# Kernel optimization log

Hardware: AMD Instinct MI355X
Metric: run time of the kernel (lower is better)

Reference implementation:

```python
import jax, jax.numpy as jnp
import numpy as np

EPS_Q = 1e-5
EPS_RMS = 1e-6


def _bitlinear(x, w):
    # absmean ternary weight quantization with STE (STE irrelevant for fwd)
    w_scale = jnp.maximum(jnp.mean(jnp.abs(w)), EPS_Q)
    w_q = jnp.clip(jnp.round(w / w_scale), -1.0, 1.0)
    w_q = jax.lax.stop_gradient(w_q - w) + w
    # per-token absmax activation quantization
    x_scale = jnp.maximum(jnp.max(jnp.abs(x), axis=-1, keepdims=True), EPS_Q)
    x_s = x / x_scale
    out = jnp.einsum('bi,oi->bo', x_s, w_q)
    return out * x_scale


def _rmsnorm(x, g):
    rms = jnp.sqrt(jnp.mean(x * x, axis=-1, keepdims=True) + EPS_RMS)
    return x / rms * g


def setup_inputs() -> dict:
    key = jax.random.key(0)
    ks = jax.random.split(key, 6)
    B, IN, H, OUT = 65536, 784, 1024, 10
    return {
        'x': jax.random.normal(ks[0], (B, IN), dtype=jnp.float32),
        'w1': jax.random.normal(ks[1], (H, IN), dtype=jnp.float32) * 0.02,
        'g1': jnp.ones((H,), dtype=jnp.float32),
        'w2': jax.random.normal(ks[2], (H, H), dtype=jnp.float32) * 0.02,
        'g2': jnp.ones((H,), dtype=jnp.float32),
        'w3': jax.random.normal(ks[3], (OUT, H), dtype=jnp.float32) * 0.02,
    }


def reference(x, w1, g1, w2, g2, w3):
    h = _bitlinear(x, w1)
    h = jax.nn.gelu(_rmsnorm(h, g1), approximate=False)
    h = _bitlinear(h, w2)
    h = jax.nn.gelu(_rmsnorm(h, g2), approximate=False)
    return _bitlinear(h, w3)
```

## Files before the change

### kernel.cpp

```cpp
#include <hip/hip_runtime.h>
#include <hip/hip_bf16.h>
#include <stdint.h>


typedef __attribute__((ext_vector_type(8))) short short8;
typedef __attribute__((ext_vector_type(4))) float f32x4;

#define B_TOTAL 65536
#define IN_DIM 784
#define IN_PAD 832
#define H_DIM 1024
#define OUT_DIM 10
#define OUT_PAD 16

__device__ __forceinline__ unsigned short f2bf(float f) {
    union { float f; unsigned u; } c; c.f = f;
    unsigned r = c.u + 0x7FFFu + ((c.u >> 16) & 1u);
    return (unsigned short)(r >> 16);
}
__device__ __forceinline__ float bf2f(unsigned short h) {
    union { unsigned u; float f; } c; c.u = ((unsigned)h) << 16;
    return c.f;
}

__device__ __forceinline__ float gelu_fast(float t) {
    const float z = t * 0.70710678118f;
    const float s = fabsf(z);
    const float tt = 1.0f / (1.0f + 0.3275911f * s);
    const float e = __expf(-s * s);
    float p = fmaf(tt, 1.061405429f, -1.453152027f);
    p = fmaf(tt, p, 1.421413741f);
    p = fmaf(tt, p, -0.284496736f);
    p = fmaf(tt, p, 0.254829592f);
    float erfa = fmaf(-p * tt, e, 1.0f);
    erfa = copysignf(erfa, z);
    return 0.5f * t * (1.0f + erfa);
}

#define GLOAD16(gp, lp)                                                        \
    __builtin_amdgcn_global_load_lds(                                          \
        (const __attribute__((address_space(1))) void*)(gp),                   \
        (__attribute__((address_space(3))) void*)(lp), 16, 0, 0)

__global__ void absum3_kernel(const float* __restrict__ w1, const float* __restrict__ w2,
                              const float* __restrict__ w3, double* acc) {
    __shared__ float red[4];
    const int which = blockIdx.y;
    const float* w = (which == 0) ? w1 : (which == 1) ? w2 : w3;
    const int n = (which == 0) ? H_DIM * IN_DIM : (which == 1) ? H_DIM * H_DIM : OUT_DIM * H_DIM;
    float s = 0.f;
    for (int i = blockIdx.x * blockDim.x + threadIdx.x; i < n; i += gridDim.x * blockDim.x)
        s += fabsf(w[i]);
#pragma unroll
    for (int o = 32; o > 0; o >>= 1) s += __shfl_xor(s, o);
    if ((threadIdx.x & 63) == 0) red[threadIdx.x >> 6] = s;
    __syncthreads();
    if (threadIdx.x == 0) {
        float t = red[0] + red[1] + red[2] + red[3];
        atomicAdd(acc + which, (double)t);
    }
}

__global__ void quant_all(const float* __restrict__ w1, const float* __restrict__ w2,
                          const float* __restrict__ w3,
                          unsigned short* __restrict__ w1q, unsigned short* __restrict__ w2q,
                          unsigned short* __restrict__ w3q, const double* sums) {
    const int k = blockIdx.x * blockDim.x + threadIdx.x;
    const int y = blockIdx.y;
    const float* w; unsigned short* wq; int o, O, K, Kp, n; const double* sum;
    if (y < 1024)      { w = w1; wq = w1q; o = y;        O = H_DIM;  K = IN_DIM; Kp = IN_PAD; n = H_DIM * IN_DIM;  sum = sums + 0; }
    else if (y < 2048) { w = w2; wq = w2q; o = y - 1024; O = H_DIM;  K = H_DIM;  Kp = H_DIM;  n = H_DIM * H_DIM;  sum = sums + 1; }
    else               { w = w3; wq = w3q; o = y - 2048; O = OUT_DIM; K = H_DIM; Kp = H_DIM;  n = OUT_DIM * H_DIM; sum = sums + 2; }
    if (k >= Kp) return;
    float scale = fmaxf((float)(*sum / (double)n), 1e-5f);
    float q = 0.f;
    if (o < O && k < K) {
        float r = rintf(w[(size_t)o * K + k] / scale);
        q = fminf(1.f, fmaxf(-1.f, r));
    }
    wq[(size_t)o * Kp + k] = f2bf(q);
}

__global__ __launch_bounds__(256)
void convert_pad(const float* __restrict__ x, unsigned short* __restrict__ xb) {
    const int g = blockIdx.x * 256 + threadIdx.x;
    const int row = g / 104;
    const int c = (g % 104) * 8;
    short8 v = 0;
    if (c < IN_DIM) {
        const float* p = x + (size_t)row * IN_DIM + c;
        float4 f0 = *(const float4*)p;
        float4 f1 = *(const float4*)(p + 4);
        v[0] = (short)f2bf(f0.x); v[1] = (short)f2bf(f0.y);
        v[2] = (short)f2bf(f0.z); v[3] = (short)f2bf(f0.w);
        v[4] = (short)f2bf(f1.x); v[5] = (short)f2bf(f1.y);
        v[6] = (short)f2bf(f1.z); v[7] = (short)f2bf(f1.w);
    }
    *(short8*)(xb + (size_t)row * IN_PAD + c) = v;
}

template<int KP>
__global__ __launch_bounds__(512, 2)
void gemm_bt(const unsigned short* __restrict__ A, const unsigned short* __restrict__ Bq,
             unsigned short* __restrict__ C) {
    constexpr int NT = KP / 64;
    __shared__ __attribute__((aligned(16))) unsigned short LDS[65536];
    const int tid = threadIdx.x;
    const int lane = tid & 63;
    const int w = tid >> 6;
    const int wm = w >> 2, wn = w & 3;
    const int lr = lane & 15, gq = lane >> 4;
    const int gsw8 = (gq ^ ((lr >> 3) << 1)) * 8;
    const int lrO = lr * 32;
    const int bid = blockIdx.x;
    const int xcd = bid & 7, slot = bid >> 3;
    const int nblk = slot & 3;
    const int mblk = xcd * (gridDim.x >> 5) + (slot >> 2);
    const int m0 = mblk * 256, n0 = nblk * 256;
    const int rS = lane >> 2;
    const int cS = ((lane & 3) ^ ((lane >> 5) << 1)) * 8;
    const int stA0 = w;
    const int stA1 = 8 + w;
    const int stB_P1 = (w >> 2) * 8 + (w & 3);
    const int stB_P3 = stB_P1 + 4;

#define STG(gbase, areaS, st)                                                  \
    {   const unsigned short* _g = (gbase) +                                   \
            (size_t)(((st) >> 1) * 16 + rS) * KP + ((st) & 1) * 32 + cS;       \
        GLOAD16(_g, &LDS[(areaS) + (st) * 512]);                               \
        GLOAD16(_g + (size_t)128 * KP, &LDS[(areaS) + (st) * 512 + 8192]); }
#define RD_A(mq, mf, kk)                                                       \
    (*(const short8*)&LDS[curS + ((wm * 8 + (mq) * 4 + (mf)) * 2 + (kk)) * 512 + lrO + gsw8])
#define RD_B(nq, nf, kk)                                                       \
    (*(const short8*)&LDS[curS + 16384 + ((wn * 4 + (nq) * 2 + (nf)) * 2 + (kk)) * 512 + lrO + gsw8])
#define MM(mq, nq, mf, nf, kk)                                                 \
    acc[(mq) * 4 + (mf)][(nq) * 2 + (nf)] =                                    \
        __builtin_amdgcn_mfma_f32_16x16x32_bf16(af[mf][kk], bf[nf][kk],        \
            acc[(mq) * 4 + (mf)][(nq) * 2 + (nf)], 0, 0, 0)

    f32x4 acc[8][4] = {};
    short8 af[4][2], bf[2][2];
    STG(A + (size_t)m0 * KP, 0, stA0);
    STG(Bq + (size_t)n0 * KP, 16384, stB_P1);
    STG(Bq + (size_t)n0 * KP, 16384, stB_P3);
    STG(A + (size_t)m0 * KP, 0, stA1);
    STG(A + (size_t)m0 * KP + 64, 32768, stA0);
    STG(Bq + (size_t)n0 * KP + 64, 49152, stB_P3);
    STG(A + (size_t)m0 * KP + 64, 32768, stA1);
    asm volatile("s_waitcnt vmcnt(6)" ::: "memory");
#pragma unroll 2
    for (int t = 0; t < NT; ++t) {
        const int curS = (t & 1) * 32768;
        const int nxtS = curS ^ 32768;
        __builtin_amdgcn_s_barrier();
        af[0][0] = RD_A(0, 0, 0); bf[0][0] = RD_B(0, 0, 0);
        af[1][0] = RD_A(0, 1, 0); bf[1][0] = RD_B(0, 1, 0);
        __builtin_amdgcn_s_setprio(1);
        MM(0, 0, 0, 0, 0); af[2][0] = RD_A(0, 2, 0);
        MM(0, 0, 0, 1, 0); af[3][0] = RD_A(0, 3, 0);
        MM(0, 0, 1, 0, 0); af[0][1] = RD_A(0, 0, 1);
        MM(0, 0, 1, 1, 0); bf[0][1] = RD_B(0, 0, 1);
        MM(0, 0, 2, 0, 0); af[1][1] = RD_A(0, 1, 1);
        MM(0, 0, 2, 1, 0); bf[1][1] = RD_B(0, 1, 1);
        MM(0, 0, 3, 0, 0); af[2][1] = RD_A(0, 2, 1);
        MM(0, 0, 3, 1, 0); af[3][1] = RD_A(0, 3, 1);
        MM(0, 0, 0, 0, 1); bf[0][0] = RD_B(1, 0, 0);
        MM(0, 0, 0, 1, 1); bf[1][0] = RD_B(1, 1, 0);
        MM(0, 0, 1, 0, 1); MM(0, 0, 1, 1, 1);
        MM(0, 0, 2, 0, 1); MM(0, 0, 2, 1, 1);
        MM(0, 0, 3, 0, 1); MM(0, 0, 3, 1, 1);
        __builtin_amdgcn_s_setprio(0);
        bf[0][1] = RD_B(1, 0, 1); bf[1][1] = RD_B(1, 1, 1);
        if (t + 1 < NT) STG(Bq + (size_t)n0 * KP + (t + 1) * 64, nxtS + 16384, stB_P1);
        __builtin_amdgcn_s_barrier();
        __builtin_amdgcn_s_setprio(1);
        MM(0, 1, 0, 0, 0); MM(0, 1, 0, 1, 0); af[0][0] = RD_A(1, 0, 0);
        MM(0, 1, 1, 0, 0); MM(0, 1, 1, 1, 0); af[1][0] = RD_A(1, 1, 0);
        MM(0, 1, 2, 0, 0); MM(0, 1, 2, 1, 0); af[2][0] = RD_A(1, 2, 0);
        MM(0, 1, 3, 0, 0); MM(0, 1, 3, 1, 0); af[3][0] = RD_A(1, 3, 0);
        MM(0, 1, 0, 0, 1); MM(0, 1, 0, 1, 1); af[0][1] = RD_A(1, 0, 1);
        MM(0, 1, 1, 0, 1); MM(0, 1, 1, 1, 1); af[1][1] = RD_A(1, 1, 1);
        MM(0, 1, 2, 0, 1); MM(0, 1, 2, 1, 1); af[2][1] = RD_A(1, 2, 1);
        MM(0, 1, 3, 0, 1); MM(0, 1, 3, 1, 1); af[3][1] = RD_A(1, 3, 1);
        __builtin_amdgcn_s_setprio(0);
        if (t + 2 < NT) STG(A + (size_t)m0 * KP + (t + 2) * 64, curS, stA0);
        __builtin_amdgcn_s_barrier();
        __builtin_amdgcn_s_setprio(1);
        MM(1, 1, 0, 0, 0); MM(1, 1, 0, 1, 0);
        MM(1, 1, 1, 0, 0); MM(1, 1, 1, 1, 0);
        MM(1, 1, 2, 0, 0); MM(1, 1, 2, 1, 0);
        MM(1, 1, 3, 0, 0); MM(1, 1, 3, 1, 0);
        MM(1, 1, 0, 0, 1); bf[0][0] = RD_B(0, 0, 0);
        MM(1, 1, 0, 1, 1); bf[1][0] = RD_B(0, 1, 0);
        MM(1, 1, 1, 0, 1); MM(1, 1, 1, 1, 1);
        MM(1, 1, 2, 0, 1); MM(1, 1, 2, 1, 1);
        MM(1, 1, 3, 0, 1); MM(1, 1, 3, 1, 1);
        __builtin_amdgcn_s_setprio(0);
        bf[0][1] = RD_B(0, 0, 1); bf[1][1] = RD_B(0, 1, 1);
        if (t + 2 < NT) STG(Bq + (size_t)n0 * KP + (t + 2) * 64, curS + 16384, stB_P3);
        __builtin_amdgcn_s_barrier();
        __builtin_amdgcn_s_setprio(1);
        MM(1, 0, 0, 0, 0); MM(1, 0, 0, 1, 0);
        MM(1, 0, 1, 0, 0); MM(1, 0, 1, 1, 0);
        MM(1, 0, 2, 0, 0); MM(1, 0, 2, 1, 0);
        MM(1, 0, 3, 0, 0); MM(1, 0, 3, 1, 0);
        MM(1, 0, 0, 0, 1); MM(1, 0, 0, 1, 1);
        MM(1, 0, 1, 0, 1); MM(1, 0, 1, 1, 1);
        MM(1, 0, 2, 0, 1); MM(1, 0, 2, 1, 1);
        MM(1, 0, 3, 0, 1); MM(1, 0, 3, 1, 1);
        __builtin_amdgcn_s_setprio(0);
        if (t + 2 < NT) STG(A + (size_t)m0 * KP + (t + 2) * 64, curS, stA1);
        if (t < NT - 2) { asm volatile("s_waitcnt vmcnt(6)" ::: "memory"); }
        else            { asm volatile("s_waitcnt vmcnt(0)" ::: "memory"); }
    }
#pragma unroll
    for (int mf = 0; mf < 8; ++mf) {
        const int grow = m0 + wm * 128 + mf * 16 + (lane >> 4) * 4;
#pragma unroll
        for (int nf = 0; nf < 4; ++nf) {
            const int gcol = n0 + wn * 64 + nf * 16 + lr;
            unsigned short* Cp = C + (size_t)grow * H_DIM + gcol;
#pragma unroll
            for (int j = 0; j < 4; ++j) Cp[(size_t)j * H_DIM] = f2bf(acc[mf][nf][j]);
        }
    }
#undef STG
#undef RD_A
#undef RD_B
#undef MM
}

__global__ __launch_bounds__(256)
void norm_gelu(const unsigned short* __restrict__ Hp, const float* __restrict__ g,
               unsigned short* __restrict__ U) {
    const int row = blockIdx.x * 4 + (threadIdx.x >> 6);
    const int lane = threadIdx.x & 63;
    const unsigned short* rp = Hp + (size_t)row * H_DIM;
    short8 v0 = *(const short8*)(rp + lane * 8);
    short8 v1 = *(const short8*)(rp + 512 + lane * 8);
    float f[16];
#pragma unroll
    for (int j = 0; j < 8; ++j) {
        f[j] = bf2f((unsigned short)v0[j]);
        f[8 + j] = bf2f((unsigned short)v1[j]);
    }
    float s = 0.f;
#pragma unroll
    for (int j = 0; j < 16; ++j) s += f[j] * f[j];
#pragma unroll
    for (int o = 32; o > 0; o >>= 1) s += __shfl_xor(s, o);
    const float rinv = 1.f / sqrtf(s * (1.f / 1024.f) + 1e-6f);
    float4 ga0 = *(const float4*)(g + lane * 8);
    float4 ga1 = *(const float4*)(g + lane * 8 + 4);
    float4 gb0 = *(const float4*)(g + 512 + lane * 8);
    float4 gb1 = *(const float4*)(g + 512 + lane * 8 + 4);
    float gv[16] = {ga0.x, ga0.y, ga0.z, ga0.w, ga1.x, ga1.y, ga1.z, ga1.w,
                    gb0.x, gb0.y, gb0.z, gb0.w, gb1.x, gb1.y, gb1.z, gb1.w};
    short8 o0, o1;
#pragma unroll
    for (int j = 0; j < 8; ++j) {
        o0[j] = (short)f2bf(gelu_fast(f[j] * rinv * gv[j]));
        o1[j] = (short)f2bf(gelu_fast(f[8 + j] * rinv * gv[8 + j]));
    }
    unsigned short* up = U + (size_t)row * H_DIM;
    *(short8*)(up + lane * 8) = o0;
    *(short8*)(up + 512 + lane * 8) = o1;
}

__global__ __launch_bounds__(256)
void norm_gelu_out(const unsigned short* __restrict__ Hp, const float* __restrict__ g,
                   const unsigned short* __restrict__ w3q, float* __restrict__ out) {
    __shared__ unsigned short Us[16][1032];
    __shared__ unsigned short Ws[16][1032];
    const int tid = threadIdx.x;
    const int lane = tid & 63, wid = tid >> 6;
    const size_t r0 = (size_t)blockIdx.x * 16;
    for (int i = tid; i < 2048; i += 256) {
        const int r = i >> 7, cg = i & 127;
        *(short8*)&Ws[r][cg * 8] = *(const short8*)(w3q + (size_t)r * H_DIM + cg * 8);
    }
    float4 ga0 = *(const float4*)(g + lane * 8);
    float4 ga1 = *(const float4*)(g + lane * 8 + 4);
    float4 gb0 = *(const float4*)(g + 512 + lane * 8);
    float4 gb1 = *(const float4*)(g + 512 + lane * 8 + 4);
    float gv[16] = {ga0.x, ga0.y, ga0.z, ga0.w, ga1.x, ga1.y, ga1.z, ga1.w,
                    gb0.x, gb0.y, gb0.z, gb0.w, gb1.x, gb1.y, gb1.z, gb1.w};
#pragma unroll
    for (int rr = 0; rr < 4; ++rr) {
        const int row = wid * 4 + rr;
        const unsigned short* rp = Hp + (r0 + row) * H_DIM;
        short8 v0 = *(const short8*)(rp + lane * 8);
        short8 v1 = *(const short8*)(rp + 512 + lane * 8);
        float f[16];
#pragma unroll
        for (int j = 0; j < 8; ++j) {
            f[j] = bf2f((unsigned short)v0[j]);
            f[8 + j] = bf2f((unsigned short)v1[j]);
        }
        float s = 0.f;
#pragma unroll
        for (int j = 0; j < 16; ++j) s += f[j] * f[j];
#pragma unroll
        for (int o = 32; o > 0; o >>= 1) s += __shfl_xor(s, o);
        const float rinv = 1.f / sqrtf(s * (1.f / 1024.f) + 1e-6f);
        short8 o0, o1;
#pragma unroll
        for (int j = 0; j < 8; ++j) {
            o0[j] = (short)f2bf(gelu_fast(f[j] * rinv * gv[j]));
            o1[j] = (short)f2bf(gelu_fast(f[8 + j] * rinv * gv[8 + j]));
        }
        *(short8*)&Us[row][lane * 8] = o0;
        *(short8*)&Us[row][512 + lane * 8] = o1;
    }
    __syncthreads();
    if (wid == 0) {
        const int lr = lane & 15, lk = (lane >> 4) * 8;
        f32x4 acc = {};
#pragma unroll
        for (int ks = 0; ks < 32; ++ks) {
            short8 a = *(const short8*)&Us[lr][ks * 32 + lk];
            short8 b = *(const short8*)&Ws[lr][ks * 32 + lk];
            acc = __builtin_amdgcn_mfma_f32_16x16x32_bf16(a, b, acc, 0, 0, 0);
        }
        if (lr < OUT_DIM) {
#pragma unroll
            for (int j = 0; j < 4; ++j)
                out[(r0 + (lane >> 4) * 4 + j) * OUT_DIM + lr] = acc[j];
        }
    }
}

extern "C" void kernel_launch(void* const* d_in, const int* in_sizes, int n_in,
                              void* d_out, int out_size, void* d_ws, size_t ws_size,
                              hipStream_t stream) {
    (void)in_sizes; (void)n_in; (void)out_size;
    const float* x  = (const float*)d_in[0];
    const float* w1 = (const float*)d_in[1];
    const float* g1 = (const float*)d_in[2];
    const float* w2 = (const float*)d_in[3];
    const float* g2 = (const float*)d_in[4];
    const float* w3 = (const float*)d_in[5];
    float* out = (float*)d_out;

    uint8_t* ws = (uint8_t*)d_ws;
    double* sums = (double*)ws;
    size_t off = 256;
    unsigned short* w1q = (unsigned short*)(ws + off); off += (size_t)H_DIM * IN_PAD * 2;
    unsigned short* w2q = (unsigned short*)(ws + off); off += (size_t)H_DIM * H_DIM * 2;
    unsigned short* w3q = (unsigned short*)(ws + off); off += (size_t)OUT_PAD * H_DIM * 2;

    size_t rem = (ws_size > off) ? ws_size - off : 0;
    int R = B_TOTAL;
    while (R > 2048 && (size_t)2 * R * H_DIM * 2 > rem) R >>= 1;
    unsigned short* bufA = (unsigned short*)(ws + off);
    unsigned short* bufB = bufA + (size_t)R * H_DIM;

    hipMemsetAsync(sums, 0, 3 * sizeof(double), stream);
    absum3_kernel<<<dim3(128, 3), 256, 0, stream>>>(w1, w2, w3, sums);
    quant_all<<<dim3(4, 2064), 256, 0, stream>>>(w1, w2, w3, w1q, w2q, w3q, sums);

    const int nchunk = B_TOTAL / R;
    for (int c = 0; c < nchunk; ++c) {
        const float* xc = x + (size_t)c * R * IN_DIM;
        convert_pad<<<R * 104 / 256, 256, 0, stream>>>(xc, bufB);
        gemm_bt<IN_PAD><<<(R / 256) * 4, 512, 0, stream>>>(bufB, w1q, bufA);
        norm_gelu<<<R / 4, 256, 0, stream>>>(bufA, g1, bufB);
        gemm_bt<H_DIM><<<(R / 256) * 4, 512, 0, stream>>>(bufB, w2q, bufA);
        norm_gelu_out<<<R / 16, 256, 0, stream>>>(bufA, g2, w3q, out + (size_t)c * R * OUT_DIM);
    }
}
```

Measured before the change: 449.8 us.

## Restructure GEMM main loop into two phases with full B fragment registers

Expands the B fragment registers to hold both N-quadrants so the four-phase loop, with four barriers per K step, collapses into two phases with two barriers. The global-to-LDS staging schedule is reorganised so each phase issues two stage loads, and the prefetch depth changes (one-ahead for some halves, two-ahead for others), with the vmcnt threshold lowered from 6 to 4. The aim is less barrier and synchronisation overhead per K tile. In exchange it uses more VGPRs for B fragments and gives less slack to hide global load latency.

```diff
diff --git a/kernel.cpp b/kernel.cpp
--- a/kernel.cpp
+++ b/kernel.cpp
@@ -121,8 +121,8 @@
     const int cS = ((lane & 3) ^ ((lane >> 5) << 1)) * 8;
     const int stA0 = w;
     const int stA1 = 8 + w;
-    const int stB_P1 = (w >> 2) * 8 + (w & 3);
-    const int stB_P3 = stB_P1 + 4;
+    const int stB0 = (w >> 2) * 8 + (w & 3);
+    const int stB1 = stB0 + 4;
 
 #define STG(gbase, areaS, st)                                                  \
     {   const unsigned short* _g = (gbase) +                                   \
@@ -135,71 +135,67 @@
     (*(const short8*)&LDS[curS + 16384 + ((wn * 4 + (nq) * 2 + (nf)) * 2 + (kk)) * 512 + lrO + gsw8])
 #define MM(mq, nq, mf, nf, kk)                                                 \
     acc[(mq) * 4 + (mf)][(nq) * 2 + (nf)] =                                    \
-        __builtin_amdgcn_mfma_f32_16x16x32_bf16(af[mf][kk], bf[nf][kk],        \
+        __builtin_amdgcn_mfma_f32_16x16x32_bf16(af[mf][kk], bf[nq][nf][kk],    \
             acc[(mq) * 4 + (mf)][(nq) * 2 + (nf)], 0, 0, 0)
 
     f32x4 acc[8][4] = {};
-    short8 af[4][2], bf[2][2];
+    short8 af[4][2], bf[2][2][2];
     STG(A + (size_t)m0 * KP, 0, stA0);
-    STG(Bq + (size_t)n0 * KP, 16384, stB_P1);
-    STG(Bq + (size_t)n0 * KP, 16384, stB_P3);
+    STG(Bq + (size_t)n0 * KP, 16384, stB0);
+    STG(Bq + (size_t)n0 * KP, 16384, stB1);
     STG(A + (size_t)m0 * KP, 0, stA1);
     STG(A + (size_t)m0 * KP + 64, 32768, stA0);
-    STG(Bq + (size_t)n0 * KP + 64, 49152, stB_P3);
-    STG(A + (size_t)m0 * KP + 64, 32768, stA1);
-    asm volatile("s_waitcnt vmcnt(6)" ::: "memory");
+    STG(Bq + (size_t)n0 * KP + 64, 49152, stB1);
+    asm volatile("s_waitcnt vmcnt(4)" ::: "memory");
 #pragma unroll 2
     for (int t = 0; t < NT; ++t) {
         const int curS = (t & 1) * 32768;
         const int nxtS = curS ^ 32768;
         __builtin_amdgcn_s_barrier();
-        af[0][0] = RD_A(0, 0, 0); bf[0][0] = RD_B(0, 0, 0);
-        af[1][0] = RD_A(0, 1, 0); bf[1][0] = RD_B(0, 1, 0);
+        af[0][0] = RD_A(0, 0, 0); bf[0][0][0] = RD_B(0, 0, 0);
+        af[1][0] = RD_A(0, 1, 0); bf[0][1][0] = RD_B(0, 1, 0);
         __builtin_amdgcn_s_setprio(1);
         MM(0, 0, 0, 0, 0); af[2][0] = RD_A(0, 2, 0);
         MM(0, 0, 0, 1, 0); af[3][0] = RD_A(0, 3, 0);
         MM(0, 0, 1, 0, 0); af[0][1] = RD_A(0, 0, 1);
-        MM(0, 0, 1, 1, 0); bf[0][1] = RD_B(0, 0, 1);
+        MM(0, 0, 1, 1, 0); bf[0][0][1] = RD_B(0, 0, 1);
         MM(0, 0, 2, 0, 0); af[1][1] = RD_A(0, 1, 1);
-        MM(0, 0, 2, 1, 0); bf[1][1] = RD_B(0, 1, 1);
+        MM(0, 0, 2, 1, 0); bf[0][1][1] = RD_B(0, 1, 1);
         MM(0, 0, 3, 0, 0); af[2][1] = RD_A(0, 2, 1);
         MM(0, 0, 3, 1, 0); af[3][1] = RD_A(0, 3, 1);
-        MM(0, 0, 0, 0, 1); bf[0][0] = RD_B(1, 0, 0);
-        MM(0, 0, 0, 1, 1); bf[1][0] = RD_B(1, 1, 0);
-        MM(0, 0, 1, 0, 1); MM(0, 0, 1, 1, 1);
+        MM(0, 0, 0, 0, 1); bf[1][0][0] = RD_B(1, 0, 0);
+        MM(0, 0, 0, 1, 1); bf[1][1][0] = RD_B(1, 1, 0);
+        MM(0, 0, 1, 0, 1); bf[1][0][1] = RD_B(1, 0, 1);
+        MM(0, 0, 1, 1, 1); bf[1][1][1] = RD_B(1, 1, 1);
         MM(0, 0, 2, 0, 1); MM(0, 0, 2, 1, 1);
         MM(0, 0, 3, 0, 1); MM(0, 0, 3, 1, 1);
+        MM(0, 1, 0, 0, 0); MM(0, 1, 0, 1, 0);
+        MM(0, 1, 1, 0, 0); MM(0, 1, 1, 1, 0);
+        MM(0, 1, 2, 0, 0); MM(0, 1, 2, 1, 0);
+        MM(0, 1, 3, 0, 0); MM(0, 1, 3, 1, 0);
+        MM(0, 1, 0, 0, 1); MM(0, 1, 0, 1, 1);
+        MM(0, 1, 1, 0, 1); MM(0, 1, 1, 1, 1);
+        MM(0, 1, 2, 0, 1); MM(0, 1, 2, 1, 1);
+        MM(0, 1, 3, 0, 1); MM(0, 1, 3, 1, 1);
         __builtin_amdgcn_s_setprio(0);
-        bf[0][1] = RD_B(1, 0, 1); bf[1][1] = RD_B(1, 1, 1);
-        if (t + 1 < NT) STG(Bq + (size_t)n0 * KP + (t + 1) * 64, nxtS + 16384, stB_P1);
-        __builtin_amdgcn_s_barrier();
-        __builtin_amdgcn_s_setprio(1);
-        MM(0, 1, 0, 0, 0); MM(0, 1, 0, 1, 0); af[0][0] = RD_A(1, 0, 0);
-        MM(0, 1, 1, 0, 0); MM(0, 1, 1, 1, 0); af[1][0] = RD_A(1, 1, 0);
-        MM(0, 1, 2, 0, 0); MM(0, 1, 2, 1, 0); af[2][0] = RD_A(1, 2, 0);
-        MM(0, 1, 3, 0, 0); MM(0, 1, 3, 1, 0); af[3][0] = RD_A(1, 3, 0);
-        MM(0, 1, 0, 0, 1); MM(0, 1, 0, 1, 1); af[0][1] = RD_A(1, 0, 1);
-        MM(0, 1, 1, 0, 1); MM(0, 1, 1, 1, 1); af[1][1] = RD_A(1, 1, 1);
-        MM(0, 1, 2, 0, 1); MM(0, 1, 2, 1, 1); af[2][1] = RD_A(1, 2, 1);
-        MM(0, 1, 3, 0, 1); MM(0, 1, 3, 1, 1); af[3][1] = RD_A(1, 3, 1);
-        __builtin_amdgcn_s_setprio(0);
-        if (t + 2 < NT) STG(A + (size_t)m0 * KP + (t + 2) * 64, curS, stA0);
+        af[0][0] = RD_A(1, 0, 0); af[1][0] = RD_A(1, 1, 0);
+        af[2][0] = RD_A(1, 2, 0); af[3][0] = RD_A(1, 3, 0);
+        af[0][1] = RD_A(1, 0, 1); af[1][1] = RD_A(1, 1, 1);
+        af[2][1] = RD_A(1, 2, 1); af[3][1] = RD_A(1, 3, 1);
+        if (t + 1 < NT) {
+            STG(Bq + (size_t)n0 * KP + (t + 1) * 64, nxtS + 16384, stB0);
+            STG(A + (size_t)m0 * KP + (t + 1) * 64, nxtS, stA1);
+        }
         __builtin_amdgcn_s_barrier();
         __builtin_amdgcn_s_setprio(1);
         MM(1, 1, 0, 0, 0); MM(1, 1, 0, 1, 0);
         MM(1, 1, 1, 0, 0); MM(1, 1, 1, 1, 0);
         MM(1, 1, 2, 0, 0); MM(1, 1, 2, 1, 0);
         MM(1, 1, 3, 0, 0); MM(1, 1, 3, 1, 0);
-        MM(1, 1, 0, 0, 1); bf[0][0] = RD_B(0, 0, 0);
-        MM(1, 1, 0, 1, 1); bf[1][0] = RD_B(0, 1, 0);
+        MM(1, 1, 0, 0, 1); MM(1, 1, 0, 1, 1);
         MM(1, 1, 1, 0, 1); MM(1, 1, 1, 1, 1);
         MM(1, 1, 2, 0, 1); MM(1, 1, 2, 1, 1);
         MM(1, 1, 3, 0, 1); MM(1, 1, 3, 1, 1);
-        __builtin_amdgcn_s_setprio(0);
-        bf[0][1] = RD_B(0, 0, 1); bf[1][1] = RD_B(0, 1, 1);
-        if (t + 2 < NT) STG(Bq + (size_t)n0 * KP + (t + 2) * 64, curS + 16384, stB_P3);
-        __builtin_amdgcn_s_barrier();
-        __builtin_amdgcn_s_setprio(1);
         MM(1, 0, 0, 0, 0); MM(1, 0, 0, 1, 0);
         MM(1, 0, 1, 0, 0); MM(1, 0, 1, 1, 0);
         MM(1, 0, 2, 0, 0); MM(1, 0, 2, 1, 0);
@@ -209,8 +205,11 @@
         MM(1, 0, 2, 0, 1); MM(1, 0, 2, 1, 1);
         MM(1, 0, 3, 0, 1); MM(1, 0, 3, 1, 1);
         __builtin_amdgcn_s_setprio(0);
-        if (t + 2 < NT) STG(A + (size_t)m0 * KP + (t + 2) * 64, curS, stA1);
-        if (t < NT - 2) { asm volatile("s_waitcnt vmcnt(6)" ::: "memory"); }
+        if (t + 2 < NT) {
+            STG(A + (size_t)m0 * KP + (t + 2) * 64, curS, stA0);
+            STG(Bq + (size_t)n0 * KP + (t + 2) * 64, curS + 16384, stB1);
+        }
+        if (t < NT - 2) { asm volatile("s_waitcnt vmcnt(4)" ::: "memory"); }
         else            { asm volatile("s_waitcnt vmcnt(0)" ::: "memory"); }
     }
 #pragma unroll
```

Measured after the change: 453.4 us. No clear change (+0.8%).

## Fuse fp32-to-bf16 input conversion into the first GEMM's A-tile loading

Applied to the files above, without the earlier changes.

Drops the separate convert_pad kernel. The first GEMM now reads fp32 x directly through registers, converts it to bf16 and writes it into swizzled LDS, with the loads interleaved with the MFMA phases. This avoids writing and re-reading a padded bf16 copy of x (about 100MB of traffic) and one launch. In exchange, each x tile is reloaded by the 4 N-blocks as fp32 (twice the bytes), the A path goes through registers rather than direct-to-LDS loads, and the extra vmcnt waits may stall the MFMA pipeline.

```diff
diff --git a/kernel.cpp b/kernel.cpp
--- a/kernel.cpp
+++ b/kernel.cpp
@@ -81,22 +81,159 @@
     wq[(size_t)o * Kp + k] = f2bf(q);
 }
 
-__global__ __launch_bounds__(256)
-void convert_pad(const float* __restrict__ x, unsigned short* __restrict__ xb) {
-    const int g = blockIdx.x * 256 + threadIdx.x;
-    const int row = g / 104;
-    const int c = (g % 104) * 8;
-    short8 v = 0;
-    if (c < IN_DIM) {
-        const float* p = x + (size_t)row * IN_DIM + c;
-        float4 f0 = *(const float4*)p;
-        float4 f1 = *(const float4*)(p + 4);
-        v[0] = (short)f2bf(f0.x); v[1] = (short)f2bf(f0.y);
-        v[2] = (short)f2bf(f0.z); v[3] = (short)f2bf(f0.w);
-        v[4] = (short)f2bf(f1.x); v[5] = (short)f2bf(f1.y);
-        v[6] = (short)f2bf(f1.z); v[7] = (short)f2bf(f1.w);
-    }
-    *(short8*)(xb + (size_t)row * IN_PAD + c) = v;
+__global__ __launch_bounds__(512, 2)
+void gemm1_x(const float* __restrict__ X, const unsigned short* __restrict__ Bq,
+             unsigned short* __restrict__ C) {
+    constexpr int NT = 13;
+    __shared__ __attribute__((aligned(16))) unsigned short LDS[65536];
+    const int tid = threadIdx.x;
+    const int lane = tid & 63;
+    const int w = tid >> 6;
+    const int wm = w >> 2, wn = w & 3;
+    const int lr = lane & 15, gq = lane >> 4;
+    const int gsw8 = (gq ^ ((lr >> 3) << 1)) * 8;
+    const int lrO = lr * 32;
+    const int bid = blockIdx.x;
+    const int xcd = bid & 7, slot = bid >> 3;
+    const int nblk = slot & 3;
+    const int mblk = xcd * (gridDim.x >> 5) + (slot >> 2);
+    const int m0 = mblk * 256, n0 = nblk * 256;
+    const int rS = lane >> 2;
+    const int cS = ((lane & 3) ^ ((lane >> 5) << 1)) * 8;
+    const int stB0 = (w >> 2) * 8 + (w & 3);
+    const int stB1 = stB0 + 4;
+    const float4 f4z = {0.f, 0.f, 0.f, 0.f};
+
+#define STGB(tt, areaS, st)                                                    \
+    {   const unsigned short* _g = Bq +                                        \
+            (size_t)(n0 + ((st) >> 1) * 16 + rS) * IN_PAD + (tt) * 64 + ((st) & 1) * 32 + cS; \
+        GLOAD16(_g, &LDS[(areaS) + (st) * 512]);                               \
+        GLOAD16(_g + (size_t)128 * IN_PAD, &LDS[(areaS) + (st) * 512 + 8192]); }
+#define ALD(s, tt, ra, rb)                                                     \
+    {   const int _gc = (tt) * 64 + ((s) & 1) * 32 + (lane & 3) * 8;           \
+        if (_gc < IN_DIM) {                                                    \
+            const float* _xp = X + (size_t)(m0 + ((s) >> 1) * 16 + (lane >> 2)) * IN_DIM + _gc; \
+            ra = *(const float4*)_xp; rb = *(const float4*)(_xp + 4);          \
+        } else { ra = f4z; rb = f4z; } }
+#define AWR(s, areaS, ra, rb)                                                  \
+    {   short8 _v;                                                             \
+        _v[0] = (short)f2bf(ra.x); _v[1] = (short)f2bf(ra.y);                  \
+        _v[2] = (short)f2bf(ra.z); _v[3] = (short)f2bf(ra.w);                  \
+        _v[4] = (short)f2bf(rb.x); _v[5] = (short)f2bf(rb.y);                  \
+        _v[6] = (short)f2bf(rb.z); _v[7] = (short)f2bf(rb.w);                  \
+        *(short8*)&LDS[(areaS) + (s) * 512 + (lane >> 2) * 32 +                \
+                       (((lane & 3) ^ ((lane >> 5) << 1)) << 3)] = _v; }
+#define RD_A(mq, mf, kk)                                                       \
+    (*(const short8*)&LDS[curS + ((wm * 8 + (mq) * 4 + (mf)) * 2 + (kk)) * 512 + lrO + gsw8])
+#define RD_B(nq, nf, kk)                                                       \
+    (*(const short8*)&LDS[curS + 16384 + ((wn * 4 + (nq) * 2 + (nf)) * 2 + (kk)) * 512 + lrO + gsw8])
+#define MM(mq, nq, mf, nf, kk)                                                 \
+    acc[(mq) * 4 + (mf)][(nq) * 2 + (nf)] =                                    \
+        __builtin_amdgcn_mfma_f32_16x16x32_bf16(af[mf][kk], bf[nf][kk],        \
+            acc[(mq) * 4 + (mf)][(nq) * 2 + (nf)], 0, 0, 0)
+
+    f32x4 acc[8][4] = {};
+    short8 af[4][2], bf[2][2];
+    float4 a0, a1, a2, a3;
+    {
+        float4 c0, c1, c2, c3;
+        ALD(w, 0, a0, a1);      ALD(w + 16, 0, a2, a3);
+        ALD(8 + w, 0, c0, c1);  ALD(24 + w, 0, c2, c3);
+        STGB(0, 16384, stB0);
+        STGB(0, 16384, stB1);
+        STGB(1, 49152, stB1);
+        asm volatile("s_waitcnt vmcnt(0)" ::: "memory");
+        AWR(w, 0, a0, a1);      AWR(w + 16, 0, a2, a3);
+        AWR(8 + w, 0, c0, c1);  AWR(24 + w, 0, c2, c3);
+        asm volatile("s_waitcnt lgkmcnt(0)" ::: "memory");
+    }
+#pragma unroll 2
+    for (int t = 0; t < NT; ++t) {
+        const int curS = (t & 1) * 32768;
+        const int nxtS = curS ^ 32768;
+        __builtin_amdgcn_s_barrier();
+        if (t + 1 < NT) { ALD(w, t + 1, a0, a1); ALD(w + 16, t + 1, a2, a3); }
+        af[0][0] = RD_A(0, 0, 0); bf[0][0] = RD_B(0, 0, 0);
+        af[1][0] = RD_A(0, 1, 0); bf[1][0] = RD_B(0, 1, 0);
+        __builtin_amdgcn_s_setprio(1);
+        MM(0, 0, 0, 0, 0); af[2][0] = RD_A(0, 2, 0);
+        MM(0, 0, 0, 1, 0); af[3][0] = RD_A(0, 3, 0);
+        MM(0, 0, 1, 0, 0); af[0][1] = RD_A(0, 0, 1);
+        MM(0, 0, 1, 1, 0); bf[0][1] = RD_B(0, 0, 1);
+        MM(0, 0, 2, 0, 0); af[1][1] = RD_A(0, 1, 1);
+        MM(0, 0, 2, 1, 0); bf[1][1] = RD_B(0, 1, 1);
+        MM(0, 0, 3, 0, 0); af[2][1] = RD_A(0, 2, 1);
+        MM(0, 0, 3, 1, 0); af[3][1] = RD_A(0, 3, 1);
+        MM(0, 0, 0, 0, 1); bf[0][0] = RD_B(1, 0, 0);
+        MM(0, 0, 0, 1, 1); bf[1][0] = RD_B(1, 1, 0);
+        MM(0, 0, 1, 0, 1); MM(0, 0, 1, 1, 1);
+        MM(0, 0, 2, 0, 1); MM(0, 0, 2, 1, 1);
+        MM(0, 0, 3, 0, 1); MM(0, 0, 3, 1, 1);
+        __builtin_amdgcn_s_setprio(0);
+        bf[0][1] = RD_B(1, 0, 1); bf[1][1] = RD_B(1, 1, 1);
+        if (t + 1 < NT) STGB(t + 1, nxtS + 16384, stB0);
+        __builtin_amdgcn_s_barrier();
+        __builtin_amdgcn_s_setprio(1);
+        MM(0, 1, 0, 0, 0); MM(0, 1, 0, 1, 0); af[0][0] = RD_A(1, 0, 0);
+        MM(0, 1, 1, 0, 0); MM(0, 1, 1, 1, 0); af[1][0] = RD_A(1, 1, 0);
+        MM(0, 1, 2, 0, 0); MM(0, 1, 2, 1, 0); af[2][0] = RD_A(1, 2, 0);
+        MM(0, 1, 3, 0, 0); MM(0, 1, 3, 1, 0); af[3][0] = RD_A(1, 3, 0);
+        MM(0, 1, 0, 0, 1); MM(0, 1, 0, 1, 1); af[0][1] = RD_A(1, 0, 1);
+        MM(0, 1, 1, 0, 1); MM(0, 1, 1, 1, 1); af[1][1] = RD_A(1, 1, 1);
+        MM(0, 1, 2, 0, 1); MM(0, 1, 2, 1, 1); af[2][1] = RD_A(1, 2, 1);
+        MM(0, 1, 3, 0, 1); MM(0, 1, 3, 1, 1); af[3][1] = RD_A(1, 3, 1);
+        __builtin_amdgcn_s_setprio(0);
+        __builtin_amdgcn_s_barrier();
+        __builtin_amdgcn_s_setprio(1);
+        MM(1, 1, 0, 0, 0); MM(1, 1, 0, 1, 0);
+        MM(1, 1, 1, 0, 0); MM(1, 1, 1, 1, 0);
+        MM(1, 1, 2, 0, 0); MM(1, 1, 2, 1, 0);
+        MM(1, 1, 3, 0, 0); MM(1, 1, 3, 1, 0);
+        MM(1, 1, 0, 0, 1); bf[0][0] = RD_B(0, 0, 0);
+        MM(1, 1, 0, 1, 1); bf[1][0] = RD_B(0, 1, 0);
+        MM(1, 1, 1, 0, 1); MM(1, 1, 1, 1, 1);
+        MM(1, 1, 2, 0, 1); MM(1, 1, 2, 1, 1);
+        MM(1, 1, 3, 0, 1); MM(1, 1, 3, 1, 1);
+        __builtin_amdgcn_s_setprio(0);
+        bf[0][1] = RD_B(0, 0, 1); bf[1][1] = RD_B(0, 1, 1);
+        asm volatile("s_waitcnt vmcnt(0)" ::: "memory");
+        if (t + 1 < NT) {
+            AWR(w, nxtS, a0, a1); AWR(w + 16, nxtS, a2, a3);
+            ALD(8 + w, t + 1, a0, a1); ALD(24 + w, t + 1, a2, a3);
+        }
+        __builtin_amdgcn_s_barrier();
+        __builtin_amdgcn_s_setprio(1);
+        MM(1, 0, 0, 0, 0); MM(1, 0, 0, 1, 0);
+        MM(1, 0, 1, 0, 0); MM(1, 0, 1, 1, 0);
+        MM(1, 0, 2, 0, 0); MM(1, 0, 2, 1, 0);
+        MM(1, 0, 3, 0, 0); MM(1, 0, 3, 1, 0);
+        MM(1, 0, 0, 0, 1); MM(1, 0, 0, 1, 1);
+        MM(1, 0, 1, 0, 1); MM(1, 0, 1, 1, 1);
+        MM(1, 0, 2, 0, 1); MM(1, 0, 2, 1, 1);
+        MM(1, 0, 3, 0, 1); MM(1, 0, 3, 1, 1);
+        __builtin_amdgcn_s_setprio(0);
+        asm volatile("s_waitcnt vmcnt(0)" ::: "memory");
+        if (t + 1 < NT) { AWR(8 + w, nxtS, a0, a1); AWR(24 + w, nxtS, a2, a3); }
+        if (t + 2 < NT) STGB(t + 2, curS + 16384, stB1);
+        asm volatile("s_waitcnt lgkmcnt(0)" ::: "memory");
+    }
+#pragma unroll
+    for (int mf = 0; mf < 8; ++mf) {
+        const int grow = m0 + wm * 128 + mf * 16 + (lane >> 4) * 4;
+#pragma unroll
+        for (int nf = 0; nf < 4; ++nf) {
+            const int gcol = n0 + wn * 64 + nf * 16 + lr;
+            unsigned short* Cp = C + (size_t)grow * H_DIM + gcol;
+#pragma unroll
+            for (int j = 0; j < 4; ++j) Cp[(size_t)j * H_DIM] = f2bf(acc[mf][nf][j]);
+        }
+    }
+#undef STGB
+#undef ALD
+#undef AWR
+#undef RD_A
+#undef RD_B
+#undef MM
 }
 
 template<int KP>
@@ -362,8 +499,7 @@
     const int nchunk = B_TOTAL / R;
     for (int c = 0; c < nchunk; ++c) {
         const float* xc = x + (size_t)c * R * IN_DIM;
-        convert_pad<<<R * 104 / 256, 256, 0, stream>>>(xc, bufB);
-        gemm_bt<IN_PAD><<<(R / 256) * 4, 512, 0, stream>>>(bufB, w1q, bufA);
+        gemm1_x<<<(R / 256) * 4, 512, 0, stream>>>(xc, w1q, bufA);
         norm_gelu<<<R / 4, 256, 0, stream>>>(bufA, g1, bufB);
         gemm_bt<H_DIM><<<(R / 256) * 4, 512, 0, stream>>>(bufB, w2q, bufA);
         norm_gelu_out<<<R / 16, 256, 0, stream>>>(bufA, g2, w3q, out + (size_t)c * R * OUT_DIM);
```

New measurement: 491.5 us. +9.3%, slower.

## Fuse second GEMM with RMSNorm, GELU and output projection in one kernel

Applied to the files above, without the earlier changes.

Replaces the second GEMM and the separate norm_gelu_out kernel with one kernel. Each block computes 64 full rows of the 1024-wide hidden output, reduces the row sums of squares across waves through LDS, then applies RMSNorm and GELU and runs the final 10-wide projection in place. This removes the write and re-read of the bf16 hidden activations to global memory. The cost is a narrow 64-row tile that reads the whole w2 matrix per block, which lowers weight reuse and leaves only 1024 blocks.

```diff
diff --git a/kernel.cpp b/kernel.cpp
--- a/kernel.cpp
+++ b/kernel.cpp
@@ -267,67 +267,123 @@
     *(short8*)(up + 512 + lane * 8) = o1;
 }
 
-__global__ __launch_bounds__(256)
-void norm_gelu_out(const unsigned short* __restrict__ Hp, const float* __restrict__ g,
-                   const unsigned short* __restrict__ w3q, float* __restrict__ out) {
-    __shared__ unsigned short Us[16][1032];
-    __shared__ unsigned short Ws[16][1032];
+__global__ __launch_bounds__(512, 2)
+void gemm2_fused(const unsigned short* __restrict__ A, const unsigned short* __restrict__ Bq,
+                 const float* __restrict__ g, const unsigned short* __restrict__ w3q,
+                 float* __restrict__ out) {
+    constexpr int NT = 32;
+    __shared__ __attribute__((aligned(16))) unsigned short LDS[69632];
     const int tid = threadIdx.x;
-    const int lane = tid & 63, wid = tid >> 6;
-    const size_t r0 = (size_t)blockIdx.x * 16;
-    for (int i = tid; i < 2048; i += 256) {
-        const int r = i >> 7, cg = i & 127;
-        *(short8*)&Ws[r][cg * 8] = *(const short8*)(w3q + (size_t)r * H_DIM + cg * 8);
-    }
-    float4 ga0 = *(const float4*)(g + lane * 8);
-    float4 ga1 = *(const float4*)(g + lane * 8 + 4);
-    float4 gb0 = *(const float4*)(g + 512 + lane * 8);
-    float4 gb1 = *(const float4*)(g + 512 + lane * 8 + 4);
-    float gv[16] = {ga0.x, ga0.y, ga0.z, ga0.w, ga1.x, ga1.y, ga1.z, ga1.w,
-                    gb0.x, gb0.y, gb0.z, gb0.w, gb1.x, gb1.y, gb1.z, gb1.w};
-#pragma unroll
-    for (int rr = 0; rr < 4; ++rr) {
-        const int row = wid * 4 + rr;
-        const unsigned short* rp = Hp + (r0 + row) * H_DIM;
-        short8 v0 = *(const short8*)(rp + lane * 8);
-        short8 v1 = *(const short8*)(rp + 512 + lane * 8);
-        float f[16];
-#pragma unroll
-        for (int j = 0; j < 8; ++j) {
-            f[j] = bf2f((unsigned short)v0[j]);
-            f[8 + j] = bf2f((unsigned short)v1[j]);
+    const int lane = tid & 63;
+    const int w = tid >> 6;
+    const int lr = lane & 15, gq = lane >> 4;
+    const int gsw8 = (gq ^ ((lr >> 3) << 1)) * 8;
+    const int lrO = lr * 32;
+    const size_t m0 = (size_t)blockIdx.x * 64;
+    const int rS = lane >> 2;
+    const int cS = ((lane & 3) ^ ((lane >> 5) << 1)) * 8;
+
+#define STAGE(t, c)                                                            \
+    {   _Pragma("unroll") for (int i = 0; i < 8; ++i) {                        \
+            const int st = w * 8 + i;                                          \
+            GLOAD16(Bq + (size_t)(st * 16 + rS) * H_DIM + (t) * 32 + cS,       \
+                    &LDS[4096 + (c) * 32768 + st * 512]);                      \
+        }                                                                      \
+        if (w < 4) GLOAD16(A + (m0 + w * 16 + rS) * H_DIM + (t) * 32 + cS,     \
+                           &LDS[(c) * 2048 + w * 512]); }
+#define RD_Af(mf) (*(const short8*)&LDS[cbuf * 2048 + (mf) * 512 + lrO + gsw8])
+#define RD_Bf(nf) (*(const short8*)&LDS[4096 + cbuf * 32768 + (8 * w + (nf)) * 512 + lrO + gsw8])
+#define FM(mf, nf)                                                             \
+    acc[mf][nf] = __builtin_amdgcn_mfma_f32_16x16x32_bf16(af[mf], bfr[nf],     \
+                                                          acc[mf][nf], 0, 0, 0)
+
+    f32x4 acc[4][8] = {};
+    short8 af[4], bfr[8];
+    STAGE(0, 0);
+    asm volatile("s_waitcnt vmcnt(0)" ::: "memory");
+    for (int t = 0; t < NT; ++t) {
+        const int cbuf = t & 1, nbuf = cbuf ^ 1;
+        __builtin_amdgcn_s_barrier();
+        if (t + 1 < NT) STAGE(t + 1, nbuf);
+        af[0] = RD_Af(0); af[1] = RD_Af(1); af[2] = RD_Af(2); af[3] = RD_Af(3);
+        bfr[0] = RD_Bf(0); bfr[1] = RD_Bf(1);
+        __builtin_amdgcn_s_setprio(1);
+        FM(0, 0); bfr[2] = RD_Bf(2);
+        FM(1, 0); bfr[3] = RD_Bf(3);
+        FM(2, 0); bfr[4] = RD_Bf(4);
+        FM(3, 0); bfr[5] = RD_Bf(5);
+        FM(0, 1); bfr[6] = RD_Bf(6);
+        FM(1, 1); bfr[7] = RD_Bf(7);
+        FM(2, 1); FM(3, 1);
+        FM(0, 2); FM(1, 2); FM(2, 2); FM(3, 2);
+        FM(0, 3); FM(1, 3); FM(2, 3); FM(3, 3);
+        FM(0, 4); FM(1, 4); FM(2, 4); FM(3, 4);
+        FM(0, 5); FM(1, 5); FM(2, 5); FM(3, 5);
+        FM(0, 6); FM(1, 6); FM(2, 6); FM(3, 6);
+        FM(0, 7); FM(1, 7); FM(2, 7); FM(3, 7);
+        __builtin_amdgcn_s_setprio(0);
+        if (t + 1 < NT) { asm volatile("s_waitcnt vmcnt(0)" ::: "memory"); }
+    }
+    __syncthreads();
+    float rs[4][4];
+#pragma unroll
+    for (int mf = 0; mf < 4; ++mf)
+#pragma unroll
+        for (int j = 0; j < 4; ++j) {
+            float s = 0.f;
+#pragma unroll
+            for (int nf = 0; nf < 8; ++nf) s += acc[mf][nf][j] * acc[mf][nf][j];
+#pragma unroll
+            for (int o = 1; o < 16; o <<= 1) s += __shfl_xor(s, o);
+            rs[mf][j] = s;
         }
-        float s = 0.f;
-#pragma unroll
-        for (int j = 0; j < 16; ++j) s += f[j] * f[j];
-#pragma unroll
-        for (int o = 32; o > 0; o >>= 1) s += __shfl_xor(s, o);
-        const float rinv = 1.f / sqrtf(s * (1.f / 1024.f) + 1e-6f);
-        short8 o0, o1;
-#pragma unroll
-        for (int j = 0; j < 8; ++j) {
-            o0[j] = (short)f2bf(gelu_fast(f[j] * rinv * gv[j]));
-            o1[j] = (short)f2bf(gelu_fast(f[8 + j] * rinv * gv[8 + j]));
+    float* red = (float*)&LDS[66048];
+    if (lr == 0) {
+#pragma unroll
+        for (int mf = 0; mf < 4; ++mf)
+#pragma unroll
+            for (int j = 0; j < 4; ++j)
+                red[(mf * 16 + gq * 4 + j) * 8 + w] = rs[mf][j];
+    }
+    __syncthreads();
+    float gcol[8];
+#pragma unroll
+    for (int nf = 0; nf < 8; ++nf) gcol[nf] = g[w * 128 + nf * 16 + lr];
+    unsigned short* Us = &LDS[0];
+#pragma unroll
+    for (int mf = 0; mf < 4; ++mf)
+#pragma unroll
+        for (int j = 0; j < 4; ++j) {
+            const int row = mf * 16 + gq * 4 + j;
+            float4 r0 = *(const float4*)&red[row * 8];
+            float4 r1 = *(const float4*)&red[row * 8 + 4];
+            float ss = r0.x + r0.y + r0.z + r0.w + r1.x + r1.y + r1.z + r1.w;
+            const float rinv = 1.f / sqrtf(ss * (1.f / 1024.f) + 1e-6f);
+#pragma unroll
+            for (int nf = 0; nf < 8; ++nf)
+                Us[row * 1032 + w * 128 + nf * 16 + lr] =
+                    f2bf(gelu_fast(acc[mf][nf][j] * rinv * gcol[nf]));
         }
-        *(short8*)&Us[row][lane * 8] = o0;
-        *(short8*)&Us[row][512 + lane * 8] = o1;
-    }
     __syncthreads();
-    if (wid == 0) {
-        const int lr = lane & 15, lk = (lane >> 4) * 8;
-        f32x4 acc = {};
-#pragma unroll
+    if (w < 4) {
+        const int lk = gq * 8;
+        f32x4 a2 = {};
+#pragma unroll 4
         for (int ks = 0; ks < 32; ++ks) {
-            short8 a = *(const short8*)&Us[lr][ks * 32 + lk];
-            short8 b = *(const short8*)&Ws[lr][ks * 32 + lk];
-            acc = __builtin_amdgcn_mfma_f32_16x16x32_bf16(a, b, acc, 0, 0, 0);
+            short8 av = *(const short8*)&Us[(w * 16 + lr) * 1032 + ks * 32 + lk];
+            short8 bv = *(const short8*)(w3q + (size_t)lr * H_DIM + ks * 32 + lk);
+            a2 = __builtin_amdgcn_mfma_f32_16x16x32_bf16(av, bv, a2, 0, 0, 0);
         }
         if (lr < OUT_DIM) {
 #pragma unroll
             for (int j = 0; j < 4; ++j)
-                out[(r0 + (lane >> 4) * 4 + j) * OUT_DIM + lr] = acc[j];
+                out[(m0 + w * 16 + gq * 4 + j) * OUT_DIM + lr] = a2[j];
         }
     }
+#undef STAGE
+#undef RD_Af
+#undef RD_Bf
+#undef FM
 }
 
 extern "C" void kernel_launch(void* const* d_in, const int* in_sizes, int n_in,
@@ -365,7 +421,7 @@
         convert_pad<<<R * 104 / 256, 256, 0, stream>>>(xc, bufB);
         gemm_bt<IN_PAD><<<(R / 256) * 4, 512, 0, stream>>>(bufB, w1q, bufA);
         norm_gelu<<<R / 4, 256, 0, stream>>>(bufA, g1, bufB);
-        gemm_bt<H_DIM><<<(R / 256) * 4, 512, 0, stream>>>(bufB, w2q, bufA);
-        norm_gelu_out<<<R / 16, 256, 0, stream>>>(bufA, g2, w3q, out + (size_t)c * R * OUT_DIM);
-    }
-}
+        gemm2_fused<<<R / 64, 512, 0, stream>>>(bufB, w2q, g2, w3q,
+                                                out + (size_t)c * R * OUT_DIM);
+    }
+}
```

Result: slower. 526.1 us (+17.0%).
